# Performance work log

Measured on AMD Instinct MI355X. Metric: run time of the kernel, lower is better.

Reference implementation:

```python
import math
import jax, jax.numpy as jnp
import numpy as np

N_EXPERTS = 8
CAPACITY_FACTOR = 1.25
AUX_COEF = 0.01  # forward passes aux_loss_coef to BOTH z-loss and lb-loss


def setup_inputs() -> dict:
    key = jax.random.key(0)
    k1, k2 = jax.random.split(key)
    B, T, D = 4, 4096, 2048
    x = jax.random.normal(k1, (B, T, D), dtype=jnp.float32)
    # nn.Linear(d_model, n_experts, bias=False) weight: (n_experts, d_model)
    W = jax.random.normal(k2, (N_EXPERTS, D), dtype=jnp.float32) * (1.0 / math.sqrt(D))
    return {"x": x, "W": W}


def reference(x, W):
    B, T, D = x.shape
    S = B * T
    E = W.shape[0]
    capacity = int(math.ceil(S / E * CAPACITY_FACTOR))  # static

    x_flat = x.reshape(S, D)
    logits = jnp.einsum("sd,ed->se", x_flat, W)          # (S, E)
    probs = jax.nn.softmax(logits, axis=-1)               # (S, E)
    gate_vals = jnp.max(probs, axis=-1)                   # (S,)
    expert_idx = jnp.argmax(probs, axis=-1)               # (S,) int

    # rank of each token within its expert's queue (token order), 0-based
    onehot = jax.nn.one_hot(expert_idx, E, dtype=jnp.int32)        # (S, E)
    rank = jnp.sum(jnp.cumsum(onehot, axis=0) * onehot, axis=-1) - 1  # (S,)
    keep = rank < capacity
    kept_gates = jnp.where(keep, gate_vals, jnp.zeros((), gate_vals.dtype))

    # z-loss: coef * mean(logsumexp(logits)^2)
    log_z = jax.scipy.special.logsumexp(logits, axis=-1)
    z_loss = AUX_COEF * jnp.mean(log_z * log_z)

    # load-balance loss: coef * E * sum(f_i * p_i)
    p = jnp.mean(probs, axis=0)                                     # (E,)
    counts = jnp.zeros((E,), dtype=probs.dtype).at[expert_idx].add(1.0)
    f = counts / S
    lb_loss = AUX_COEF * E * jnp.sum(f * p)

    aux_loss = z_loss + lb_loss
    return expert_idx, kept_gates, aux_loss
```

## Files before the change

### kernel.cpp

```cpp
#include <hip/hip_runtime.h>

#define S_TOKENS 16384
#define DMODEL   2048
#define NE       8
#define CAPACITY 2560
#define AUXC     0.01f


__global__ __launch_bounds__(512, 4) void logits_kernel(
    const float* __restrict__ x, const float* __restrict__ W,
    int* __restrict__ idx_out, float* __restrict__ gate_out,
    float* __restrict__ bsums) {
    __shared__ float4 WE[NE * 512];

    const int tid  = threadIdx.x;
    const int wave = tid >> 6;
    const int lane = tid & 63;

    {
        const float4* __restrict__ Wf4 = (const float4*)W;
        #pragma unroll
        for (int i = 0; i < 8; ++i) WE[i * 512 + tid] = Wf4[i * 512 + tid];
    }
    __syncthreads();

    const int t0 = blockIdx.x * 32 + wave * 4;
    const float4* __restrict__ xr0 = (const float4*)x + (size_t)(t0 + 0) * (DMODEL / 4);
    const float4* __restrict__ xr1 = (const float4*)x + (size_t)(t0 + 1) * (DMODEL / 4);
    const float4* __restrict__ xr2 = (const float4*)x + (size_t)(t0 + 2) * (DMODEL / 4);
    const float4* __restrict__ xr3 = (const float4*)x + (size_t)(t0 + 3) * (DMODEL / 4);

    float acc[4][NE];
    #pragma unroll
    for (int t = 0; t < 4; ++t) {
        #pragma unroll
        for (int e = 0; e < NE; ++e) acc[t][e] = 0.0f;
    }

    #pragma unroll 2
    for (int it = 0; it < (DMODEL / 4) / 64; ++it) {
        const int j = it * 64 + lane;
        float4 xv0 = xr0[j];
        float4 xv1 = xr1[j];
        float4 xv2 = xr2[j];
        float4 xv3 = xr3[j];
        #pragma unroll
        for (int e = 0; e < NE; ++e) {
            float4 w = WE[e * 512 + j];
            acc[0][e] += xv0.x * w.x + xv0.y * w.y + xv0.z * w.z + xv0.w * w.w;
            acc[1][e] += xv1.x * w.x + xv1.y * w.y + xv1.z * w.z + xv1.w * w.w;
            acc[2][e] += xv2.x * w.x + xv2.y * w.y + xv2.z * w.z + xv2.w * w.w;
            acc[3][e] += xv3.x * w.x + xv3.y * w.y + xv3.z * w.z + xv3.w * w.w;
        }
    }

    const int  eL = lane >> 3;
    const bool b5 = (lane & 32) != 0;
    const bool b4 = (lane & 16) != 0;
    const bool b3 = (lane & 8)  != 0;

    float pacc = 0.0f;
    float zacc = 0.0f;

    #pragma unroll
    for (int t = 0; t < 4; ++t) {
        float b[4];
        #pragma unroll
        for (int i = 0; i < 4; ++i) {
            float keepv = b5 ? acc[t][i + 4] : acc[t][i];
            float sendv = b5 ? acc[t][i]     : acc[t][i + 4];
            b[i] = keepv + __shfl_xor(sendv, 32);
        }
        float c[2];
        #pragma unroll
        for (int i = 0; i < 2; ++i) {
            float keepv = b4 ? b[i + 2] : b[i];
            float sendv = b4 ? b[i]     : b[i + 2];
            c[i] = keepv + __shfl_xor(sendv, 16);
        }
        float keepv = b3 ? c[1] : c[0];
        float sendv = b3 ? c[0] : c[1];
        float d = keepv + __shfl_xor(sendv, 8);
        d += __shfl_xor(d, 1);
        d += __shfl_xor(d, 2);
        d += __shfl_xor(d, 4);

        float m = d;
        m = fmaxf(m, __shfl_xor(m, 8));
        m = fmaxf(m, __shfl_xor(m, 16));
        m = fmaxf(m, __shfl_xor(m, 32));
        int cand = (d == m) ? eL : NE;
        cand = min(cand, __shfl_xor(cand, 8));
        cand = min(cand, __shfl_xor(cand, 16));
        cand = min(cand, __shfl_xor(cand, 32));
        float p = expf(d - m);
        float z = p;
        z += __shfl_xor(z, 8);
        z += __shfl_xor(z, 16);
        z += __shfl_xor(z, 32);
        float gate = 1.0f / z;

        if ((lane & 7) == 0) pacc += p * gate;
        if (lane == 0) {
            const int token = t0 + t;
            idx_out[token]  = cand;
            gate_out[token] = gate;
            float lz = m + logf(z);
            zacc += lz * lz;
        }
    }

    __syncthreads();
    float* red = (float*)WE;
    float* zrd = (float*)WE + 64;
    if ((lane & 7) == 0) red[wave * 8 + eL] = pacc;
    if (lane == 0)       zrd[wave] = zacc;
    __syncthreads();
    if (tid < NE) {
        float s = 0.0f;
        #pragma unroll
        for (int w = 0; w < 8; ++w) s += red[w * 8 + tid];
        bsums[blockIdx.x * 12 + tid] = s;
    } else if (tid == NE) {
        float s = 0.0f;
        #pragma unroll
        for (int w = 0; w < 8; ++w) s += zrd[w];
        bsums[blockIdx.x * 12 + NE] = s;
    }
}

__global__ __launch_bounds__(256, 1) void scan_kernel(
    const int* __restrict__ idx, int* __restrict__ prefix,
    const float* __restrict__ bsums, float* __restrict__ aux_out) {
    __shared__ int   arr[NE][256];
    __shared__ float bs[9][256];
    __shared__ float ptot[9];
    const int t = threadIdx.x;

    #pragma unroll
    for (int q = 0; q < 9; ++q)
        bs[q][t] = bsums[t * 12 + q] + bsums[(t + 256) * 12 + q];

    unsigned clo = 0, chi = 0;
    const int4* __restrict__ idx4 = (const int4*)idx;
    #pragma unroll 4
    for (int i = 0; i < 16; ++i) {
        int4 v = idx4[t * 16 + i];
        if (v.x < 4) clo += 1u << (8 * v.x); else chi += 1u << (8 * (v.x - 4));
        if (v.y < 4) clo += 1u << (8 * v.y); else chi += 1u << (8 * (v.y - 4));
        if (v.z < 4) clo += 1u << (8 * v.z); else chi += 1u << (8 * (v.z - 4));
        if (v.w < 4) clo += 1u << (8 * v.w); else chi += 1u << (8 * (v.w - 4));
    }
    int cnt[8];
    cnt[0] = clo & 255; cnt[1] = (clo >> 8) & 255; cnt[2] = (clo >> 16) & 255; cnt[3] = clo >> 24;
    cnt[4] = chi & 255; cnt[5] = (chi >> 8) & 255; cnt[6] = (chi >> 16) & 255; cnt[7] = chi >> 24;
    #pragma unroll
    for (int e = 0; e < NE; ++e) arr[e][t] = cnt[e];
    __syncthreads();

    if (t < 64) {
        float s[9];
        #pragma unroll
        for (int q = 0; q < 9; ++q)
            s[q] = bs[q][t] + bs[q][t + 64] + bs[q][t + 128] + bs[q][t + 192];
        #pragma unroll
        for (int off = 32; off > 0; off >>= 1) {
            #pragma unroll
            for (int q = 0; q < 9; ++q) s[q] += __shfl_xor(s[q], off);
        }
        if (t == 0) {
            #pragma unroll
            for (int q = 0; q < 9; ++q) ptot[q] = s[q];
        }
    }

    for (int off = 1; off < 256; off <<= 1) {
        int v[8];
        #pragma unroll
        for (int e = 0; e < NE; ++e) v[e] = (t >= off) ? arr[e][t - off] : 0;
        __syncthreads();
        #pragma unroll
        for (int e = 0; e < NE; ++e) arr[e][t] += v[e];
        __syncthreads();
    }
    #pragma unroll
    for (int e = 0; e < NE; ++e) prefix[t * 8 + e] = arr[e][t] - cnt[e];

    if (t == 0) {
        float lb = 0.0f;
        #pragma unroll
        for (int e = 0; e < NE; ++e) {
            float f = (float)arr[e][255] / (float)S_TOKENS;
            float p = ptot[e] / (float)S_TOKENS;
            lb += f * p;
        }
        lb *= AUXC * (float)NE;
        float zl = AUXC * (ptot[8] / (float)S_TOKENS);
        aux_out[0] = zl + lb;
    }
}

__global__ __launch_bounds__(64, 1) void output_kernel(
    const int* __restrict__ idx, const float* __restrict__ gate,
    const int* __restrict__ prefix, float* __restrict__ out) {
    const int b = blockIdx.x;
    const int l = threadIdx.x;
    const int token = b * 64 + l;
    const int e = idx[token];

    unsigned long long mymask = 0;
    #pragma unroll
    for (int q = 0; q < NE; ++q) {
        unsigned long long msk = __ballot(e == q);
        if (e == q) mymask = msk;
    }
    unsigned long long lt = (1ull << l) - 1ull;
    int rank = prefix[b * 8 + e] + __popcll(mymask & lt);

    out[token] = (float)e;
    out[S_TOKENS + token] = (rank < CAPACITY) ? gate[token] : 0.0f;
}

extern "C" void kernel_launch(void* const* d_in, const int* in_sizes, int n_in,
                              void* d_out, int out_size, void* d_ws, size_t ws_size,
                              hipStream_t stream) {
    const float* x = (const float*)d_in[0];
    const float* W = (const float*)d_in[1];
    float* out = (float*)d_out;

    int*   ws_idx    = (int*)d_ws;
    float* ws_gate   = (float*)d_ws + 16384;
    int*   ws_prefix = (int*)d_ws + 32768;
    float* ws_bsums  = (float*)d_ws + 34816;

    logits_kernel<<<512, 512, 0, stream>>>(x, W, ws_idx, ws_gate, ws_bsums);
    scan_kernel<<<1, 256, 0, stream>>>(ws_idx, ws_prefix, ws_bsums, out + 2 * S_TOKENS);
    output_kernel<<<256, 64, 0, stream>>>(ws_idx, ws_gate, ws_prefix, out);
}
```

Baseline: 205.2 us.

## Fuse scan and output kernels into one single-block finalize kernel with wave-shuffle scan

Merges the scan and output kernels into a single 1024-thread finalize kernel. Each thread handles 16 tokens, builds packed 16-bit per-expert counts, and computes exclusive prefixes with wave shuffle scans plus a small cross-wave scan. That replaces the shared-memory Hillis-Steele loop with its many barriers, and drops one launch and the prefix round trip through memory. The logits kernel now writes each wave's four idx and gate values as single vector stores. The cost is that all output writing runs on one block, which limits parallelism for the final pass.

After: 203.3 us. Within noise of the previous version (-0.9%).

```diff
diff --git a/kernel.cpp b/kernel.cpp
--- a/kernel.cpp
+++ b/kernel.cpp
@@ -61,6 +61,8 @@
 
     float pacc = 0.0f;
     float zacc = 0.0f;
+    int4   ei = make_int4(0, 0, 0, 0);
+    float4 gv = make_float4(0.f, 0.f, 0.f, 0.f);
 
     #pragma unroll
     for (int t = 0; t < 4; ++t) {
@@ -102,12 +104,17 @@
 
         if ((lane & 7) == 0) pacc += p * gate;
         if (lane == 0) {
-            const int token = t0 + t;
-            idx_out[token]  = cand;
-            gate_out[token] = gate;
+            if (t == 0) { ei.x = cand; gv.x = gate; }
+            if (t == 1) { ei.y = cand; gv.y = gate; }
+            if (t == 2) { ei.z = cand; gv.z = gate; }
+            if (t == 3) { ei.w = cand; gv.w = gate; }
             float lz = m + logf(z);
             zacc += lz * lz;
         }
+    }
+    if (lane == 0) {
+        ((int4*)idx_out)[blockIdx.x * 8 + wave]    = ei;
+        ((float4*)gate_out)[blockIdx.x * 8 + wave] = gv;
     }
 
     __syncthreads();
@@ -129,96 +136,138 @@
     }
 }
 
-__global__ __launch_bounds__(256, 1) void scan_kernel(
-    const int* __restrict__ idx, int* __restrict__ prefix,
-    const float* __restrict__ bsums, float* __restrict__ aux_out) {
-    __shared__ int   arr[NE][256];
-    __shared__ float bs[9][256];
-    __shared__ float ptot[9];
-    const int t = threadIdx.x;
-
+__global__ __launch_bounds__(1024, 1) void finalize_kernel(
+    const int* __restrict__ idx, const float* __restrict__ gate,
+    const float* __restrict__ bsums, float* __restrict__ out) {
+    __shared__ float    bs[9][256];
+    __shared__ unsigned wtot[16][4];
+    __shared__ unsigned wexc[16][4];
+    __shared__ unsigned gtot[4];
+    __shared__ float    ptot[9];
+
+    const int t    = threadIdx.x;
+    const int wave = t >> 6;
+    const int lane = t & 63;
+
+    if (t < 256) {
+        #pragma unroll
+        for (int q = 0; q < 9; ++q)
+            bs[q][t] = bsums[t * 12 + q] + bsums[(t + 256) * 12 + q];
+    }
+
+    const int4* __restrict__ idx4 = (const int4*)idx;
+    int4 v0 = idx4[t * 4 + 0];
+    int4 v1 = idx4[t * 4 + 1];
+    int4 v2 = idx4[t * 4 + 2];
+    int4 v3 = idx4[t * 4 + 3];
+    unsigned clo = 0, chi = 0;
+#define HACC(E) { int e_ = (E); if (e_ < 4) clo += 1u << (e_ * 8); else chi += 1u << ((e_ - 4) * 8); }
+    HACC(v0.x) HACC(v0.y) HACC(v0.z) HACC(v0.w)
+    HACC(v1.x) HACC(v1.y) HACC(v1.z) HACC(v1.w)
+    HACC(v2.x) HACC(v2.y) HACC(v2.z) HACC(v2.w)
+    HACC(v3.x) HACC(v3.y) HACC(v3.z) HACC(v3.w)
+#undef HACC
+    unsigned p01 = (clo & 0xFFu)         | ((clo >> 8) & 0xFFu) << 16;
+    unsigned p23 = ((clo >> 16) & 0xFFu) | ((clo >> 24)       ) << 16;
+    unsigned p45 = (chi & 0xFFu)         | ((chi >> 8) & 0xFFu) << 16;
+    unsigned p67 = ((chi >> 16) & 0xFFu) | ((chi >> 24)       ) << 16;
+
+    unsigned i01 = p01, i23 = p23, i45 = p45, i67 = p67;
     #pragma unroll
-    for (int q = 0; q < 9; ++q)
-        bs[q][t] = bsums[t * 12 + q] + bsums[(t + 256) * 12 + q];
-
-    unsigned clo = 0, chi = 0;
-    const int4* __restrict__ idx4 = (const int4*)idx;
-    #pragma unroll 4
-    for (int i = 0; i < 16; ++i) {
-        int4 v = idx4[t * 16 + i];
-        if (v.x < 4) clo += 1u << (8 * v.x); else chi += 1u << (8 * (v.x - 4));
-        if (v.y < 4) clo += 1u << (8 * v.y); else chi += 1u << (8 * (v.y - 4));
-        if (v.z < 4) clo += 1u << (8 * v.z); else chi += 1u << (8 * (v.z - 4));
-        if (v.w < 4) clo += 1u << (8 * v.w); else chi += 1u << (8 * (v.w - 4));
-    }
-    int cnt[8];
-    cnt[0] = clo & 255; cnt[1] = (clo >> 8) & 255; cnt[2] = (clo >> 16) & 255; cnt[3] = clo >> 24;
-    cnt[4] = chi & 255; cnt[5] = (chi >> 8) & 255; cnt[6] = (chi >> 16) & 255; cnt[7] = chi >> 24;
-    #pragma unroll
-    for (int e = 0; e < NE; ++e) arr[e][t] = cnt[e];
-    __syncthreads();
-
-    if (t < 64) {
+    for (int off = 1; off < 64; off <<= 1) {
+        unsigned u01 = __shfl_up(i01, off);
+        unsigned u23 = __shfl_up(i23, off);
+        unsigned u45 = __shfl_up(i45, off);
+        unsigned u67 = __shfl_up(i67, off);
+        if (lane >= off) { i01 += u01; i23 += u23; i45 += u45; i67 += u67; }
+    }
+    if (lane == 63) {
+        wtot[wave][0] = i01; wtot[wave][1] = i23;
+        wtot[wave][2] = i45; wtot[wave][3] = i67;
+    }
+    __syncthreads();
+
+    if (wave == 0) {
+        const int k = lane >> 4;
+        const int w = lane & 15;
+        unsigned val = wtot[w][k];
+        unsigned inc = val;
+        #pragma unroll
+        for (int off = 1; off < 16; off <<= 1) {
+            unsigned u = __shfl_up(inc, off, 16);
+            if (w >= off) inc += u;
+        }
+        wexc[w][k] = inc - val;
+        if (w == 15) gtot[k] = inc;
+    } else if (wave == 1) {
         float s[9];
         #pragma unroll
         for (int q = 0; q < 9; ++q)
-            s[q] = bs[q][t] + bs[q][t + 64] + bs[q][t + 128] + bs[q][t + 192];
+            s[q] = bs[q][lane] + bs[q][lane + 64] + bs[q][lane + 128] + bs[q][lane + 192];
         #pragma unroll
         for (int off = 32; off > 0; off >>= 1) {
             #pragma unroll
             for (int q = 0; q < 9; ++q) s[q] += __shfl_xor(s[q], off);
         }
-        if (t == 0) {
+        if (lane == 0) {
             #pragma unroll
             for (int q = 0; q < 9; ++q) ptot[q] = s[q];
         }
     }
-
-    for (int off = 1; off < 256; off <<= 1) {
-        int v[8];
-        #pragma unroll
-        for (int e = 0; e < NE; ++e) v[e] = (t >= off) ? arr[e][t - off] : 0;
-        __syncthreads();
-        #pragma unroll
-        for (int e = 0; e < NE; ++e) arr[e][t] += v[e];
-        __syncthreads();
-    }
-    #pragma unroll
-    for (int e = 0; e < NE; ++e) prefix[t * 8 + e] = arr[e][t] - cnt[e];
+    __syncthreads();
 
     if (t == 0) {
         float lb = 0.0f;
         #pragma unroll
         for (int e = 0; e < NE; ++e) {
-            float f = (float)arr[e][255] / (float)S_TOKENS;
+            float cnt_e = (float)((gtot[e >> 1] >> ((e & 1) * 16)) & 0xFFFFu);
+            float f = cnt_e / (float)S_TOKENS;
             float p = ptot[e] / (float)S_TOKENS;
             lb += f * p;
         }
         lb *= AUXC * (float)NE;
         float zl = AUXC * (ptot[8] / (float)S_TOKENS);
-        aux_out[0] = zl + lb;
-    }
-}
-
-__global__ __launch_bounds__(64, 1) void output_kernel(
-    const int* __restrict__ idx, const float* __restrict__ gate,
-    const int* __restrict__ prefix, float* __restrict__ out) {
-    const int b = blockIdx.x;
-    const int l = threadIdx.x;
-    const int token = b * 64 + l;
-    const int e = idx[token];
-
-    unsigned long long mymask = 0;
-    #pragma unroll
-    for (int q = 0; q < NE; ++q) {
-        unsigned long long msk = __ballot(e == q);
-        if (e == q) mymask = msk;
-    }
-    unsigned long long lt = (1ull << l) - 1ull;
-    int rank = prefix[b * 8 + e] + __popcll(mymask & lt);
-
-    out[token] = (float)e;
-    out[S_TOKENS + token] = (rank < CAPACITY) ? gate[token] : 0.0f;
+        out[2 * S_TOKENS] = zl + lb;
+    }
+
+    const unsigned b01 = wexc[wave][0] + (i01 - p01);
+    const unsigned b23 = wexc[wave][1] + (i23 - p23);
+    const unsigned b45 = wexc[wave][2] + (i45 - p45);
+    const unsigned b67 = wexc[wave][3] + (i67 - p67);
+
+    const float4* __restrict__ gate4 = (const float4*)gate;
+    float4 g0 = gate4[t * 4 + 0];
+    float4 g1 = gate4[t * 4 + 1];
+    float4 g2 = gate4[t * 4 + 2];
+    float4 g3 = gate4[t * 4 + 3];
+
+    unsigned llo = 0, lhi = 0;
+    float4 e0, e1, e2, e3, q0, q1, q2, q3;
+#define STEP(EV, GV, OE, OG) { \
+    int e_ = (EV); \
+    unsigned pw_ = (e_ < 4) ? ((e_ < 2) ? b01 : b23) : ((e_ < 6) ? b45 : b67); \
+    int base_  = (int)((pw_ >> ((e_ & 1) * 16)) & 0xFFFFu); \
+    int local_ = (int)(((e_ < 4) ? (llo >> (e_ * 8)) : (lhi >> ((e_ - 4) * 8))) & 0xFFu); \
+    if (e_ < 4) llo += 1u << (e_ * 8); else lhi += 1u << ((e_ - 4) * 8); \
+    OE = (float)e_; \
+    OG = ((base_ + local_) < CAPACITY) ? (GV) : 0.0f; \
+}
+    STEP(v0.x, g0.x, e0.x, q0.x) STEP(v0.y, g0.y, e0.y, q0.y)
+    STEP(v0.z, g0.z, e0.z, q0.z) STEP(v0.w, g0.w, e0.w, q0.w)
+    STEP(v1.x, g1.x, e1.x, q1.x) STEP(v1.y, g1.y, e1.y, q1.y)
+    STEP(v1.z, g1.z, e1.z, q1.z) STEP(v1.w, g1.w, e1.w, q1.w)
+    STEP(v2.x, g2.x, e2.x, q2.x) STEP(v2.y, g2.y, e2.y, q2.y)
+    STEP(v2.z, g2.z, e2.z, q2.z) STEP(v2.w, g2.w, e2.w, q2.w)
+    STEP(v3.x, g3.x, e3.x, q3.x) STEP(v3.y, g3.y, e3.y, q3.y)
+    STEP(v3.z, g3.z, e3.z, q3.z) STEP(v3.w, g3.w, e3.w, q3.w)
+#undef STEP
+
+    float4* __restrict__ oute = (float4*)out;
+    float4* __restrict__ outg = (float4*)(out + S_TOKENS);
+    oute[t * 4 + 0] = e0; oute[t * 4 + 1] = e1;
+    oute[t * 4 + 2] = e2; oute[t * 4 + 3] = e3;
+    outg[t * 4 + 0] = q0; outg[t * 4 + 1] = q1;
+    outg[t * 4 + 2] = q2; outg[t * 4 + 3] = q3;
 }
 
 extern "C" void kernel_launch(void* const* d_in, const int* in_sizes, int n_in,
@@ -228,12 +277,10 @@
     const float* W = (const float*)d_in[1];
     float* out = (float*)d_out;
 
-    int*   ws_idx    = (int*)d_ws;
-    float* ws_gate   = (float*)d_ws + 16384;
-    int*   ws_prefix = (int*)d_ws + 32768;
-    float* ws_bsums  = (float*)d_ws + 34816;
+    int*   ws_idx   = (int*)d_ws;
+    float* ws_gate  = (float*)d_ws + 16384;
+    float* ws_bsums = (float*)d_ws + 34816;
 
     logits_kernel<<<512, 512, 0, stream>>>(x, W, ws_idx, ws_gate, ws_bsums);
-    scan_kernel<<<1, 256, 0, stream>>>(ws_idx, ws_prefix, ws_bsums, out + 2 * S_TOKENS);
-    output_kernel<<<256, 64, 0, stream>>>(ws_idx, ws_gate, ws_prefix, out);
-}
+    finalize_kernel<<<1, 1024, 0, stream>>>(ws_idx, ws_gate, ws_bsums, out);
+}
```
